# Kernel optimization log

Measured on AMD Instinct MI355X. Metric: run time of the kernel, lower is better.

Reference implementation:

```python
import jax, jax.numpy as jnp
import numpy as np

B, S, D, H = 4, 2048, 512, 8
DH = D // H


def setup_inputs() -> dict:
    key = jax.random.key(0)
    ks = jax.random.split(key, 7)
    scale = 1.0 / np.sqrt(DH)  # mimic nn.Linear init magnitude
    return {
        "x": jax.random.normal(ks[0], (B, S, D), dtype=jnp.float32),
        "Wq": jax.random.normal(ks[1], (H, DH, DH), dtype=jnp.float32) * scale,
        "bq": jax.random.normal(ks[2], (H, DH), dtype=jnp.float32) * scale,
        "Wk": jax.random.normal(ks[3], (H, DH, DH), dtype=jnp.float32) * scale,
        "bk": jax.random.normal(ks[4], (H, DH), dtype=jnp.float32) * scale,
        "Wv": jax.random.normal(ks[5], (H, DH, DH), dtype=jnp.float32) * scale,
        "bv": jax.random.normal(ks[6], (H, DH), dtype=jnp.float32) * scale,
    }


def reference(x, Wq, bq, Wk, bk, Wv, bv):
    # x: [B, S, D] -> per-head slices [B, S, H, DH] (contiguous chunks, as in torch slicing)
    xh = x.reshape(B, S, H, DH)
    # nn.Linear: y = x @ W.T + b, per head. Wq[h] is [out, in].
    q = jnp.einsum("bshd,hed->bshe", xh, Wq) + bq  # [B, S, H, DH]
    k = jnp.einsum("bshd,hed->bshe", xh, Wk) + bk
    v = jnp.einsum("bshd,hed->bshe", xh, Wv) + bv
    scores = jnp.einsum("bshe,bthe->bhst", q, k) / jnp.sqrt(jnp.float32(DH))  # [B, H, S, S]
    attn = jax.nn.softmax(scores, axis=-1)
    out = jnp.einsum("bhst,bthe->bshe", attn, v)  # [B, S, H, DH]
    return out.reshape(B, S, D)  # hstack of head outputs == concat along feature dim
```

## Files before the change

kernel.cpp:

```cpp
#include <hip/hip_runtime.h>
#include <math.h>

#define B_ 4
#define S_ 2048
#define D_ 512
#define H_ 8
#define DH_ 64
#define BH_ (B_*H_)
#define SCALE 0.1803368801111243f

typedef __attribute__((ext_vector_type(4)))  float f32x4;
typedef __attribute__((ext_vector_type(16))) float f32x16;
typedef __attribute__((ext_vector_type(8)))  short bf16x8;
typedef __attribute__((ext_vector_type(4)))  uint  u32x4;

__device__ inline uint rnepk(float a, float b) {
    uint ua = __builtin_bit_cast(uint, a), ub = __builtin_bit_cast(uint, b);
    ua += 0x7FFFu + ((ua >> 16) & 1u);
    ub += 0x7FFFu + ((ub >> 16) & 1u);
    return (ua >> 16) | (ub & 0xFFFF0000u);
}
__device__ inline uint truncpk(float lo, float hi) {
    return __builtin_amdgcn_perm(__builtin_bit_cast(uint, hi),
                                 __builtin_bit_cast(uint, lo), 0x07060302u);
}
__device__ inline f32x16 zero16() {
    f32x16 z;
    #pragma unroll
    for (int i = 0; i < 16; ++i) z[i] = 0.f;
    return z;
}
__device__ inline bf16x8 pack8(f32x4 a, f32x4 c) {
    u32x4 u;
    u.x = rnepk(a[0], a[1]); u.y = rnepk(a[2], a[3]);
    u.z = rnepk(c[0], c[1]); u.w = rnepk(c[2], c[3]);
    return __builtin_bit_cast(bf16x8, u);
}

#if __has_builtin(__builtin_amdgcn_permlane32_swap)
__device__ inline void lane32swap(uint& a, uint& b) {
    typedef __attribute__((ext_vector_type(2))) uint u32x2;
    u32x2 r = __builtin_amdgcn_permlane32_swap(a, b, false, false);
    a = r.x; b = r.y;
}
#else
__device__ inline void lane32swap(uint& a, uint& b) {
    const int l5 = (threadIdx.x & 63) >> 5;
    uint send = l5 ? a : b;
    uint recv = __shfl_xor(send, 32);
    uint an = l5 ? recv : a;
    uint bn = l5 ? b : recv;
    a = an; b = bn;
}
#endif

__device__ inline void dma16(const ushort* g, ushort* l) {
    __builtin_amdgcn_global_load_lds(
        (const __attribute__((address_space(1))) unsigned int*)g,
        (__attribute__((address_space(3))) unsigned int*)l, 16, 0, 0);
}

__global__ __launch_bounds__(256, 2)
void qkv_mfma(const float* __restrict__ x,
              const float* __restrict__ Wq, const float* __restrict__ bq,
              const float* __restrict__ Wk, const float* __restrict__ bk,
              const float* __restrict__ Wv, const float* __restrict__ bv,
              ushort* __restrict__ Qf, ushort* __restrict__ Kf,
              ushort* __restrict__ Vf)
{
    const int bh = blockIdx.x, b = bh >> 3, h = bh & 7;
    const int sblk = blockIdx.y, s0 = sblk * 128;
    const int tid = threadIdx.x;
    const int w = tid >> 6, lane = tid & 63, l31 = lane & 31, l5 = lane >> 5;

    __shared__ __align__(16) ushort bnc[4][2560];
    __shared__ __align__(16) ushort vsh[64 * 136];
    ushort* mybnc = bnc[w];

    const int srow = w * 32 + l31;
    const float* xr = x + ((size_t)(b * S_ + s0 + srow)) * D_ + h * DH_;
    bf16x8 xf[4];
    #pragma unroll
    for (int st = 0; st < 4; ++st)
        xf[st] = pack8(*(const f32x4*)(xr + st * 16 + l5 * 8),
                       *(const f32x4*)(xr + st * 16 + l5 * 8 + 4));

    {
        bf16x8 wf[2][4];
        #pragma unroll
        for (int et = 0; et < 2; ++et) {
            const float* wr = Wk + h * DH_ * DH_ + (et * 32 + l31) * DH_;
            #pragma unroll
            for (int st = 0; st < 4; ++st)
                wf[et][st] = pack8(*(const f32x4*)(wr + st * 16 + l5 * 8),
                                   *(const f32x4*)(wr + st * 16 + l5 * 8 + 4));
        }
        #pragma unroll
        for (int et = 0; et < 2; ++et) {
            f32x16 acc = zero16();
            #pragma unroll
            for (int st = 0; st < 4; ++st)
                acc = __builtin_amdgcn_mfma_f32_32x32x16_bf16(wf[et][st], xf[st], acc, 0, 0, 0);
            #pragma unroll
            for (int rg = 0; rg < 4; ++rg) {
                float4 b4 = *(const float4*)(bk + h * DH_ + et * 32 + rg * 8 + l5 * 4);
                uint2 pk;
                pk.x = rnepk(acc[rg * 4 + 0] + b4.x, acc[rg * 4 + 1] + b4.y);
                pk.y = rnepk(acc[rg * 4 + 2] + b4.z, acc[rg * 4 + 3] + b4.w);
                *(uint2*)(mybnc + l31 * 72 + et * 32 + rg * 8 + l5 * 4) = pk;
            }
        }
        const int kt = sblk * 2 + (w >> 1), g = w & 1;
        ushort* kd = Kf + (((size_t)(bh * 32 + kt)) * 2 + g) * 2048;
        #pragma unroll
        for (int st = 0; st < 4; ++st) {
            uint4 v = *(const uint4*)(mybnc + l31 * 72 + st * 16 + l5 * 8);
            *(uint4*)(kd + st * 512 + lane * 8) = v;
        }
    }

    {
        bf16x8 wf[2][4];
        #pragma unroll
        for (int et = 0; et < 2; ++et) {
            const float* wr = Wq + h * DH_ * DH_ + (et * 32 + l31) * DH_;
            #pragma unroll
            for (int st = 0; st < 4; ++st)
                wf[et][st] = pack8(*(const f32x4*)(wr + st * 16 + l5 * 8),
                                   *(const f32x4*)(wr + st * 16 + l5 * 8 + 4));
        }
        #pragma unroll
        for (int et = 0; et < 2; ++et) {
            f32x16 acc = zero16();
            #pragma unroll
            for (int st = 0; st < 4; ++st)
                acc = __builtin_amdgcn_mfma_f32_32x32x16_bf16(wf[et][st], xf[st], acc, 0, 0, 0);
            #pragma unroll
            for (int rg = 0; rg < 4; ++rg) {
                float4 b4 = *(const float4*)(bq + h * DH_ + et * 32 + rg * 8 + l5 * 4);
                uint2 pk;
                pk.x = rnepk((acc[rg * 4 + 0] + b4.x) * SCALE, (acc[rg * 4 + 1] + b4.y) * SCALE);
                pk.y = rnepk((acc[rg * 4 + 2] + b4.z) * SCALE, (acc[rg * 4 + 3] + b4.w) * SCALE);
                *(uint2*)(mybnc + l31 * 72 + et * 32 + rg * 8 + l5 * 4) = pk;
            }
        }
        ushort* qd = Qf + ((size_t)(bh * 64 + sblk * 4 + w)) * 2048;
        #pragma unroll
        for (int st = 0; st < 4; ++st) {
            uint4 v = *(const uint4*)(mybnc + l31 * 72 + st * 16 + l5 * 8);
            *(uint4*)(qd + st * 512 + lane * 8) = v;
        }
    }

    {
        bf16x8 wf[2][4];
        #pragma unroll
        for (int et = 0; et < 2; ++et) {
            const float* wr = Wv + h * DH_ * DH_ + (et * 32 + l31) * DH_;
            #pragma unroll
            for (int st = 0; st < 4; ++st)
                wf[et][st] = pack8(*(const f32x4*)(wr + st * 16 + l5 * 8),
                                   *(const f32x4*)(wr + st * 16 + l5 * 8 + 4));
        }
        #pragma unroll
        for (int et = 0; et < 2; ++et) {
            f32x16 acc = zero16();
            #pragma unroll
            for (int st = 0; st < 4; ++st)
                acc = __builtin_amdgcn_mfma_f32_32x32x16_bf16(xf[st], wf[et][st], acc, 0, 0, 0);
            const float bb = bv[h * DH_ + et * 32 + l31];
            #pragma unroll
            for (int rg = 0; rg < 4; ++rg) {
                uint2 pk;
                pk.x = rnepk(acc[rg * 4 + 0] + bb, acc[rg * 4 + 1] + bb);
                pk.y = rnepk(acc[rg * 4 + 2] + bb, acc[rg * 4 + 3] + bb);
                *(uint2*)(vsh + (et * 32 + l31) * 136 + w * 32 + rg * 8 + l5 * 4) = pk;
            }
        }
        __syncthreads();
        #pragma unroll
        for (int i = 0; i < 4; ++i) {
            const int c = w * 4 + i;
            const int ktl = c >> 3, dht = (c >> 2) & 1, st = c & 3;
            uint4 v = *(const uint4*)(vsh + (dht * 32 + l31) * 136 + ktl * 64 + st * 16 + l5 * 8);
            *(uint4*)(Vf + (((size_t)(bh * 32 + sblk * 2 + ktl)) * 2 + dht) * 2048
                      + st * 512 + lane * 8) = v;
        }
    }
}

__global__ __launch_bounds__(256, 2)
void flash_mfma(const ushort* __restrict__ Qf, const ushort* __restrict__ Kf,
                const ushort* __restrict__ Vf, float* __restrict__ out)
{
    const int blk = blockIdx.x;
    const int bh = blk & 31, qblk = blk >> 5;
    const int b = bh >> 3, h = bh & 7;
    const int tid = threadIdx.x;
    const int w = tid >> 6, lane = tid & 63, l31 = lane & 31, l5 = lane >> 5;
    const int p = w >> 1, qh = w & 1;

    __shared__ __align__(16) ushort lds_u[32768];

    const ushort* kvsrc = (w & 1) ? (Vf + (size_t)bh * 32 * 4096)
                                  : (Kf + (size_t)bh * 32 * 4096);

    {
        const ushort* gb = kvsrc + (size_t)p * 4096;
        ushort* ld = lds_u + w * 4096;
        #pragma unroll
        for (int i = 0; i < 8; ++i)
            dma16(gb + i * 512 + lane * 8, ld + i * 512);
    }

    bf16x8 qf[2][4];
    #pragma unroll
    for (int qt = 0; qt < 2; ++qt)
        #pragma unroll
        for (int st = 0; st < 4; ++st)
            qf[qt][st] = *(const bf16x8*)(Qf + ((size_t)(bh * 64 + qblk * 4 + qh * 2 + qt)) * 2048
                                          + st * 512 + lane * 8);

    f32x16 O[2][2];
    #pragma unroll
    for (int i = 0; i < 2; ++i)
        #pragma unroll
        for (int j = 0; j < 2; ++j) O[i][j] = zero16();
    float lsum[2] = {0.f, 0.f};

    for (int step = 0; step < 16; ++step) {
        __syncthreads();
        ushort* cbuf = lds_u + (step & 1) * 16384;
        if (step < 15) {
            const ushort* gb = kvsrc + (size_t)(2 * (step + 1) + p) * 4096;
            ushort* ld = lds_u + ((step + 1) & 1) * 16384 + w * 4096;
            #pragma unroll
            for (int i = 0; i < 8; ++i)
                dma16(gb + i * 512 + lane * 8, ld + i * 512);
        }
        const ushort* kreg = cbuf + p * 8192;
        const ushort* vreg = kreg + 4096;

        bf16x8 pf[2][4];
        #pragma unroll
        for (int g = 0; g < 2; ++g) {
            bf16x8 kf[4];
            #pragma unroll
            for (int st = 0; st < 4; ++st)
                kf[st] = *(const bf16x8*)(kreg + (g * 4 + st) * 512 + lane * 8);
            #pragma unroll
            for (int qt = 0; qt < 2; ++qt) {
                f32x16 sc_ = zero16();
                #pragma unroll
                for (int st = 0; st < 4; ++st)
                    sc_ = __builtin_amdgcn_mfma_f32_32x32x16_bf16(kf[st], qf[qt][st], sc_, 0, 0, 0);
                uint pr[8];
                #pragma unroll
                for (int rg = 0; rg < 4; ++rg) {
                    float p0 = __builtin_amdgcn_exp2f(sc_[rg * 4 + 0]);
                    float p1 = __builtin_amdgcn_exp2f(sc_[rg * 4 + 1]);
                    float p2 = __builtin_amdgcn_exp2f(sc_[rg * 4 + 2]);
                    float p3 = __builtin_amdgcn_exp2f(sc_[rg * 4 + 3]);
                    lsum[qt] += (p0 + p1) + (p2 + p3);
                    pr[2 * rg + 0] = truncpk(p0, p1);
                    pr[2 * rg + 1] = truncpk(p2, p3);
                }
                #pragma unroll
                for (int pp = 0; pp < 2; ++pp) {
                    lane32swap(pr[4 * pp + 0], pr[4 * pp + 2]);
                    lane32swap(pr[4 * pp + 1], pr[4 * pp + 3]);
                    u32x4 u; u.x = pr[4 * pp + 0]; u.y = pr[4 * pp + 1];
                    u.z = pr[4 * pp + 2]; u.w = pr[4 * pp + 3];
                    pf[qt][g * 2 + pp] = __builtin_bit_cast(bf16x8, u);
                }
            }
        }

        #pragma unroll
        for (int dht = 0; dht < 2; ++dht) {
            bf16x8 vf[4];
            #pragma unroll
            for (int st = 0; st < 4; ++st)
                vf[st] = *(const bf16x8*)(vreg + (dht * 4 + st) * 512 + lane * 8);
            #pragma unroll
            for (int qt = 0; qt < 2; ++qt)
                #pragma unroll
                for (int st = 0; st < 4; ++st)
                    O[dht][qt] = __builtin_amdgcn_mfma_f32_32x32x16_bf16(vf[st], pf[qt][st],
                                                                          O[dht][qt], 0, 0, 0);
        }
    }

    #pragma unroll
    for (int qt = 0; qt < 2; ++qt) lsum[qt] += __shfl_xor(lsum[qt], 32);

    __syncthreads();
    float* mb = (float*)lds_u;
    float* reg = mb + qh * 4352;
    float* lsA = mb + 2 * 4352;

    if (p == 1) {
        #pragma unroll
        for (int dht = 0; dht < 2; ++dht)
            #pragma unroll
            for (int qt = 0; qt < 2; ++qt)
                #pragma unroll
                for (int rg = 0; rg < 4; ++rg) {
                    f32x4 v4;
                    v4[0] = O[dht][qt][rg * 4 + 0];
                    v4[1] = O[dht][qt][rg * 4 + 1];
                    v4[2] = O[dht][qt][rg * 4 + 2];
                    v4[3] = O[dht][qt][rg * 4 + 3];
                    *(f32x4*)(reg + (qt * 32 + l31) * 68 + dht * 32 + rg * 8 + l5 * 4) = v4;
                }
        if (l5 == 0) {
            #pragma unroll
            for (int qt = 0; qt < 2; ++qt)
                lsA[qh * 64 + qt * 32 + l31] = lsum[qt];
        }
    }
    __syncthreads();
    if (p == 0) {
        float linv[2];
        #pragma unroll
        for (int qt = 0; qt < 2; ++qt)
            linv[qt] = 1.0f / (lsum[qt] + lsA[qh * 64 + qt * 32 + l31]);
        #pragma unroll
        for (int dht = 0; dht < 2; ++dht)
            #pragma unroll
            for (int qt = 0; qt < 2; ++qt)
                #pragma unroll
                for (int rg = 0; rg < 4; ++rg) {
                    float* a = reg + (qt * 32 + l31) * 68 + dht * 32 + rg * 8 + l5 * 4;
                    f32x4 part = *(const f32x4*)a;
                    f32x4 v4;
                    v4[0] = (O[dht][qt][rg * 4 + 0] + part[0]) * linv[qt];
                    v4[1] = (O[dht][qt][rg * 4 + 1] + part[1]) * linv[qt];
                    v4[2] = (O[dht][qt][rg * 4 + 2] + part[2]) * linv[qt];
                    v4[3] = (O[dht][qt][rg * 4 + 3] + part[3]) * linv[qt];
                    *(f32x4*)a = v4;
                }
    }
    __syncthreads();

    const int q0 = qblk * 128;
    #pragma unroll
    for (int i = 0; i < 8; ++i) {
        const int slot = tid + 256 * i;
        const int r = slot >> 4, c = slot & 15;
        f32x4 v = *(const f32x4*)(mb + (r >> 6) * 4352 + (r & 63) * 68 + c * 4);
        *(f32x4*)(out + ((size_t)(b * S_ + q0 + r)) * D_ + h * DH_ + c * 4) = v;
    }
}

extern "C" void kernel_launch(void* const* d_in, const int* in_sizes, int n_in,
                              void* d_out, int out_size, void* d_ws, size_t ws_size,
                              hipStream_t stream) {
    const float* x  = (const float*)d_in[0];
    const float* Wq = (const float*)d_in[1];
    const float* bq = (const float*)d_in[2];
    const float* Wk = (const float*)d_in[3];
    const float* bk = (const float*)d_in[4];
    const float* Wv = (const float*)d_in[5];
    const float* bv = (const float*)d_in[6];
    float* outp = (float*)d_out;

    ushort* Qf = (ushort*)d_ws;
    ushort* Kf = Qf + (size_t)BH_ * S_ * DH_;
    ushort* Vf = Kf + (size_t)BH_ * S_ * DH_;

    qkv_mfma<<<dim3(BH_, S_ / 128), 256, 0, stream>>>(x, Wq, bq, Wk, bk, Wv, bv,
                                                      Qf, Kf, Vf);
    flash_mfma<<<dim3(32 * 16), 256, 0, stream>>>(Qf, Kf, Vf, outp);
}
```

Before: 130.0 us.

## Pre-pack projection weights to bf16 fragments and raise MFMA wave priority

Adds a small prep kernel that converts the Q/K/V weights to bf16 once, in MFMA fragment order, so the QKV projection kernel loads ready fragments instead of every block re-reading fp32 weights and packing them. The flash attention loop also raises wave priority around its MFMA bursts with s_setprio, aiming for better interleaving of matrix and exp/ALU work across waves. The cost is an extra kernel launch and workspace space for the packed weights.

```diff
diff --git a/kernel.cpp b/kernel.cpp
--- a/kernel.cpp
+++ b/kernel.cpp
@@ -60,11 +60,29 @@
         (__attribute__((address_space(3))) unsigned int*)l, 16, 0, 0);
 }
 
+__global__ __launch_bounds__(256)
+void prep_w(const float* __restrict__ Wq, const float* __restrict__ Wk,
+            const float* __restrict__ Wv, ushort* __restrict__ Wf)
+{
+    const int pb = blockIdx.x;
+    const int proj = pb >> 3, h = pb & 7;
+    const float* W = (proj == 0 ? Wq : proj == 1 ? Wk : Wv) + h * DH_ * DH_;
+    #pragma unroll
+    for (int it = 0; it < 2; ++it) {
+        const int slot = threadIdx.x + it * 256;
+        const int c = slot >> 6, lane = slot & 63;
+        const int l31 = lane & 31, l5 = lane >> 5;
+        const int et = c >> 2, st = c & 3;
+        const float* wr = W + (et * 32 + l31) * DH_ + st * 16 + l5 * 8;
+        bf16x8 v = pack8(*(const f32x4*)wr, *(const f32x4*)(wr + 4));
+        *(bf16x8*)(Wf + ((size_t)pb * 8 + c) * 512 + lane * 8) = v;
+    }
+}
+
 __global__ __launch_bounds__(256, 2)
 void qkv_mfma(const float* __restrict__ x,
-              const float* __restrict__ Wq, const float* __restrict__ bq,
-              const float* __restrict__ Wk, const float* __restrict__ bk,
-              const float* __restrict__ Wv, const float* __restrict__ bv,
+              const float* __restrict__ bq, const float* __restrict__ bk,
+              const float* __restrict__ bv, const ushort* __restrict__ Wf,
               ushort* __restrict__ Qf, ushort* __restrict__ Kf,
               ushort* __restrict__ Vf)
 {
@@ -77,6 +95,10 @@
     __shared__ __align__(16) ushort vsh[64 * 136];
     ushort* mybnc = bnc[w];
 
+    const ushort* wqb = Wf + ((size_t)(0 * 8 + h)) * 8 * 512;
+    const ushort* wkb = Wf + ((size_t)(1 * 8 + h)) * 8 * 512;
+    const ushort* wvb = Wf + ((size_t)(2 * 8 + h)) * 8 * 512;
+
     const int srow = w * 32 + l31;
     const float* xr = x + ((size_t)(b * S_ + s0 + srow)) * D_ + h * DH_;
     bf16x8 xf[4];
@@ -88,13 +110,10 @@
     {
         bf16x8 wf[2][4];
         #pragma unroll
-        for (int et = 0; et < 2; ++et) {
-            const float* wr = Wk + h * DH_ * DH_ + (et * 32 + l31) * DH_;
-            #pragma unroll
-            for (int st = 0; st < 4; ++st)
-                wf[et][st] = pack8(*(const f32x4*)(wr + st * 16 + l5 * 8),
-                                   *(const f32x4*)(wr + st * 16 + l5 * 8 + 4));
-        }
+        for (int et = 0; et < 2; ++et)
+            #pragma unroll
+            for (int st = 0; st < 4; ++st)
+                wf[et][st] = *(const bf16x8*)(wkb + (et * 4 + st) * 512 + lane * 8);
         #pragma unroll
         for (int et = 0; et < 2; ++et) {
             f32x16 acc = zero16();
@@ -122,13 +141,10 @@
     {
         bf16x8 wf[2][4];
         #pragma unroll
-        for (int et = 0; et < 2; ++et) {
-            const float* wr = Wq + h * DH_ * DH_ + (et * 32 + l31) * DH_;
-            #pragma unroll
-            for (int st = 0; st < 4; ++st)
-                wf[et][st] = pack8(*(const f32x4*)(wr + st * 16 + l5 * 8),
-                                   *(const f32x4*)(wr + st * 16 + l5 * 8 + 4));
-        }
+        for (int et = 0; et < 2; ++et)
+            #pragma unroll
+            for (int st = 0; st < 4; ++st)
+                wf[et][st] = *(const bf16x8*)(wqb + (et * 4 + st) * 512 + lane * 8);
         #pragma unroll
         for (int et = 0; et < 2; ++et) {
             f32x16 acc = zero16();
@@ -155,13 +171,10 @@
     {
         bf16x8 wf[2][4];
         #pragma unroll
-        for (int et = 0; et < 2; ++et) {
-            const float* wr = Wv + h * DH_ * DH_ + (et * 32 + l31) * DH_;
-            #pragma unroll
-            for (int st = 0; st < 4; ++st)
-                wf[et][st] = pack8(*(const f32x4*)(wr + st * 16 + l5 * 8),
-                                   *(const f32x4*)(wr + st * 16 + l5 * 8 + 4));
-        }
+        for (int et = 0; et < 2; ++et)
+            #pragma unroll
+            for (int st = 0; st < 4; ++st)
+                wf[et][st] = *(const bf16x8*)(wvb + (et * 4 + st) * 512 + lane * 8);
         #pragma unroll
         for (int et = 0; et < 2; ++et) {
             f32x16 acc = zero16();
@@ -251,9 +264,11 @@
             #pragma unroll
             for (int qt = 0; qt < 2; ++qt) {
                 f32x16 sc_ = zero16();
+                __builtin_amdgcn_s_setprio(1);
                 #pragma unroll
                 for (int st = 0; st < 4; ++st)
                     sc_ = __builtin_amdgcn_mfma_f32_32x32x16_bf16(kf[st], qf[qt][st], sc_, 0, 0, 0);
+                __builtin_amdgcn_s_setprio(0);
                 uint pr[8];
                 #pragma unroll
                 for (int rg = 0; rg < 4; ++rg) {
@@ -282,12 +297,14 @@
             #pragma unroll
             for (int st = 0; st < 4; ++st)
                 vf[st] = *(const bf16x8*)(vreg + (dht * 4 + st) * 512 + lane * 8);
+            __builtin_amdgcn_s_setprio(1);
             #pragma unroll
             for (int qt = 0; qt < 2; ++qt)
                 #pragma unroll
                 for (int st = 0; st < 4; ++st)
                     O[dht][qt] = __builtin_amdgcn_mfma_f32_32x32x16_bf16(vf[st], pf[qt][st],
                                                                           O[dht][qt], 0, 0, 0);
+            __builtin_amdgcn_s_setprio(0);
         }
     }
 
@@ -368,8 +385,10 @@
     ushort* Qf = (ushort*)d_ws;
     ushort* Kf = Qf + (size_t)BH_ * S_ * DH_;
     ushort* Vf = Kf + (size_t)BH_ * S_ * DH_;
-
-    qkv_mfma<<<dim3(BH_, S_ / 128), 256, 0, stream>>>(x, Wq, bq, Wk, bk, Wv, bv,
+    ushort* Wfb = Vf + (size_t)BH_ * S_ * DH_;
+
+    prep_w<<<dim3(24), 256, 0, stream>>>(Wq, Wk, Wv, Wfb);
+    qkv_mfma<<<dim3(BH_, S_ / 128), 256, 0, stream>>>(x, bq, bk, bv, Wfb,
                                                       Qf, Kf, Vf);
     flash_mfma<<<dim3(32 * 16), 256, 0, stream>>>(Qf, Kf, Vf, outp);
 }
```

Result: faster. 125.2 us (-3.7%).
